# Optimization experiments

Hardware: AMD Instinct MI355X
Metric: run time of the kernel (lower is better)

Reference implementation:

```python
import jax, jax.numpy as jnp
import numpy as np

B, N, G = 1, 8192, 512      # batch, n_cells, n_genes
D_DEN = 512                  # denoise hidden
D_EMB1, D_EMB = 256, 32      # embed hidden / final embed dim
D_Q = 64                     # quality hidden
H = 4                        # interaction heads
LBD = 1.0


def _lin_init(key, fan_in, fan_out):
    # torch nn.Linear default init (uniform +/- 1/sqrt(fan_in)); stored as [in,out]
    k1, k2 = jax.random.split(key)
    bound = 1.0 / np.sqrt(fan_in)
    W = jax.random.uniform(k1, (fan_in, fan_out), minval=-bound, maxval=bound, dtype=jnp.float32)
    b = jax.random.uniform(k2, (fan_out,), minval=-bound, maxval=bound, dtype=jnp.float32)
    return W, b


def setup_inputs() -> dict:
    key = jax.random.key(0)
    ks = jax.random.split(key, 9)
    raw_expr = jax.random.normal(ks[0], (B, N, G), dtype=jnp.float32)
    dW1, db1 = _lin_init(ks[1], G, D_DEN)
    dW2, db2 = _lin_init(ks[2], D_DEN, G)
    eW1, eb1 = _lin_init(ks[3], G, D_EMB1)
    eW2, eb2 = _lin_init(ks[4], D_EMB1, D_EMB)
    qW1, qb1 = _lin_init(ks[5], G, D_Q)
    qW2, qb2 = _lin_init(ks[6], D_Q, 1)
    # CellInteract.transform: xavier_normal -> std = sqrt(2/(d+d)) = 1/sqrt(d)
    transforms = jax.random.normal(ks[7], (H, D_EMB, D_EMB), dtype=jnp.float32) * np.float32(1.0 / np.sqrt(D_EMB))
    # gene_response is a trained parameter (zeros at init); random so path is non-trivial
    gene_responses = jax.random.normal(ks[8], (H, G, G), dtype=jnp.float32) * np.float32(0.02)
    return dict(raw_expr=raw_expr, dW1=dW1, db1=db1, dW2=dW2, db2=db2,
                eW1=eW1, eb1=eb1, eW2=eW2, eb2=eb2,
                qW1=qW1, qb1=qb1, qW2=qW2, qb2=qb2,
                transforms=transforms, gene_responses=gene_responses)


def _cdist(x):
    # pairwise euclidean distance over cells: [B,N,D] -> [B,N,N], grad-safe at 0
    sq = jnp.sum(x * x, axis=-1)
    d2 = sq[..., :, None] + sq[..., None, :] - 2.0 * jnp.einsum('bnd,bmd->bnm', x, x)
    d2 = jnp.maximum(d2, 0.0)
    eps = 1e-12
    safe = jnp.where(d2 > eps, d2, eps)
    return jnp.where(d2 > eps, jnp.sqrt(safe), 0.0)


def reference(raw_expr, dW1, db1, dW2, db2, eW1, eb1, eW2, eb2,
              qW1, qb1, qW2, qb2, transforms, gene_responses):
    # CellDenoise: Linear-Tanh-Linear + residual
    denoised = jnp.tanh(raw_expr @ dW1 + db1) @ dW2 + db2 + raw_expr      # [B,N,G]
    # CellQualify: Linear-Tanh-Linear -> [B,N,1]
    quality = jnp.tanh(raw_expr @ qW1 + qb1) @ qW2 + qb2
    # CellEmbed: Linear-Tanh-Linear -> [B,N,D_EMB]
    enc = jnp.tanh(raw_expr @ eW1 + eb1) @ eW2 + eb2
    # CellSmooth: softmax(-cdist + quality^T) @ denoised
    scores = -_cdist(enc) + jnp.swapaxes(quality, -1, -2)                 # [B,N,N]
    sim = jax.nn.softmax(scores, axis=-1)
    smoothed = sim @ denoised                                             # [B,N,G]
    # CellInteract heads (interact=True path): sigmoid(enc T enc^T) @ expr @ gene_response / N
    inter = jnp.zeros_like(smoothed)
    for h in range(H):
        ci = jax.nn.sigmoid(jnp.einsum('bnd,de,bme->bnm', enc, transforms[h], enc))
        inter = inter + (ci @ smoothed) @ gene_responses[h] / N
    final = smoothed + LBD * inter
    return denoised, smoothed, final
```

## Files before the change

kernel.cpp:

```cpp
#include <hip/hip_runtime.h>
#include <hip/hip_bf16.h>
#include <stdint.h>
#if !__has_builtin(__builtin_amdgcn_cvt_pk_fp8_f32)
#include <hip/hip_fp8.h>
#endif

#define NC 8192
#define GG 512

typedef __attribute__((ext_vector_type(8))) short bf16x8;
typedef __attribute__((ext_vector_type(4))) float fx4;
typedef __attribute__((ext_vector_type(4))) unsigned int uint4v;
typedef __attribute__((ext_vector_type(2))) long long llx2;

__device__ __forceinline__ float bf2f(short s){
  union { uint32_t u; float f; } c; c.u = ((uint32_t)(uint16_t)s) << 16; return c.f;
}
__device__ __forceinline__ short f2bf(float f){
  union { float f; uint32_t u; } c; c.f = f;
  uint32_t u = c.u;
  uint32_t r = (u + 0x7fffu + ((u >> 16) & 1u)) >> 16;
  return (short)(uint16_t)r;
}
__device__ __forceinline__ uint32_t au(float f){
  union { float f; uint32_t u; } c; c.f = f; return c.u;
}
#if __has_builtin(__builtin_amdgcn_rcpf)
__device__ __forceinline__ float fast_rcp(float x){ return __builtin_amdgcn_rcpf(x); }
#else
__device__ __forceinline__ float fast_rcp(float x){ return 1.0f / x; }
#endif
#if __has_builtin(__builtin_amdgcn_sqrtf)
__device__ __forceinline__ float fast_sqrt(float x){ return __builtin_amdgcn_sqrtf(x); }
#else
__device__ __forceinline__ float fast_sqrt(float x){ return sqrtf(x); }
#endif
__device__ __forceinline__ float tanh_fast(float x){
  float e = __expf(2.0f * x);
  return 1.0f - 2.0f * fast_rcp(e + 1.0f);
}
__device__ __forceinline__ uint32_t pack_bf(float lo, float hi){
  return __builtin_amdgcn_perm(au(hi) + 0x8000u, au(lo) + 0x8000u, 0x07060302u);
}
template<bool HI>
__device__ __forceinline__ uint32_t pk_fp8(float a, float b, uint32_t old){
#if __has_builtin(__builtin_amdgcn_cvt_pk_fp8_f32)
  return (uint32_t)__builtin_amdgcn_cvt_pk_fp8_f32(a, b, (int)old, HI);
#else
  __hip_fp8_e4m3 fa(a), fb(b);
  uint32_t v = (uint32_t)fa.__x | ((uint32_t)fb.__x << 8);
  return HI ? ((old & 0x0000ffffu) | (v << 16)) : ((old & 0xffff0000u) | v);
#endif
}
__device__ __forceinline__ void g2l16(const void* g, void* l){
  __builtin_amdgcn_global_load_lds((const __attribute__((address_space(1))) void*)g,
                                   (__attribute__((address_space(3))) void*)l, 16, 0, 0);
}

__global__ void cast_f32_bf16(const float* __restrict__ in, short* __restrict__ out, int n){
  int i = (blockIdx.x * 256 + threadIdx.x) * 4;
  if (i < n){
    float4 v = *(const float4*)(in + i);
    uint32_t lo = (uint32_t)(uint16_t)f2bf(v.x) | ((uint32_t)(uint16_t)f2bf(v.y) << 16);
    uint32_t hi = (uint32_t)(uint16_t)f2bf(v.z) | ((uint32_t)(uint16_t)f2bf(v.w) << 16);
    *(uint2*)(out + i) = make_uint2(lo, hi);
  }
}

__global__ void transpose_cast(const float* __restrict__ in, short* __restrict__ out,
                               int R, int C, int ostride, int roff, int permute){
  __shared__ float t[32][33];
  int c0 = blockIdx.x * 32, r0 = blockIdx.y * 32;
  int x = threadIdx.x & 31, y = threadIdx.x >> 5;
  #pragma unroll
  for (int it = 0; it < 4; ++it)
    t[y + 8*it][x] = in[(size_t)(r0 + y + 8*it) * C + c0 + x];
  __syncthreads();
  int xp = permute ? (((x >> 2) & 3) * 8 + ((x >> 4) & 1) * 4 + (x & 3)) : x;
  #pragma unroll
  for (int it = 0; it < 4; ++it)
    out[(size_t)(c0 + y + 8*it) * ostride + roff + r0 + xp] = f2bf(t[x][y + 8*it]);
}

__global__ void transpose_cast8(const float* __restrict__ in, unsigned char* __restrict__ out,
                                int C, int ostride){
  __shared__ float t[32][33];
  int c0 = blockIdx.x * 32, r0 = blockIdx.y * 32;
  int x = threadIdx.x & 31, y = threadIdx.x >> 5;
  #pragma unroll
  for (int it = 0; it < 4; ++it)
    t[y + 8*it][x] = in[(size_t)(r0 + y + 8*it) * C + c0 + x];
  __syncthreads();
  int xp = ((x >> 2) & 3) * 16 + ((r0 >> 5) & 1) * 8 + ((x >> 4) & 1) * 4 + (x & 3);
  int cb = r0 & ~63;
  #pragma unroll
  for (int it = 0; it < 4; ++it){
    float v = t[x][y + 8*it];
    out[(size_t)(c0 + y + 8*it) * ostride + cb + xp] =
        (unsigned char)(pk_fp8<false>(v, v, 0u) & 0xffu);
  }
}

__global__ void fill_bias(const float* __restrict__ db1, const float* __restrict__ eb1,
                          const float* __restrict__ qb1, float* __restrict__ b){
  int i = blockIdx.x * 256 + threadIdx.x;
  if (i >= 896) return;
  float v = 0.0f;
  if (i < 512) v = db1[i];
  else if (i < 768) v = eb1[i - 512];
  else if (i < 832) v = qb1[i - 768];
  b[i] = v;
}

__global__ __launch_bounds__(256, 2)
void gemm_bt(const short* __restrict__ A, int lda, const short* __restrict__ B, int ldb,
             int K, int mode, const float* __restrict__ bias,
             const float* __restrict__ res, int ldres,
             float* __restrict__ outf, short* __restrict__ outb, int ldo, float scale)
{
  __shared__ __align__(16) short As[64 * 64];
  __shared__ __align__(16) short Bs[128 * 64];
  const int tid = threadIdx.x;
  const int lane = tid & 63, wave = tid >> 6;
  const int wm = wave >> 1, wn = wave & 1;
  const int l16 = lane & 15, q = lane >> 4;
  const size_t i0 = (size_t)blockIdx.y * 64;
  const int n0 = blockIdx.x * 128;
  fx4 acc[2][4] = {};

  for (int k0 = 0; k0 < K; k0 += 64){
    #pragma unroll
    for (int inst = 0; inst < 2; ++inst){
      int ch = inst * 256 + tid;
      int r = ch >> 3, pc = ch & 7;
      int colc = (pc ^ (r & 7)) * 8;
      g2l16(A + (i0 + r) * (size_t)lda + k0 + colc, As + ch * 8);
    }
    #pragma unroll
    for (int inst = 0; inst < 4; ++inst){
      int ch = inst * 256 + tid;
      int r = ch >> 3, pc = ch & 7;
      int colc = (pc ^ (r & 7)) * 8;
      g2l16(B + (size_t)(n0 + r) * (size_t)ldb + k0 + colc, Bs + ch * 8);
    }
    __syncthreads();
    #pragma unroll
    for (int ks = 0; ks < 2; ++ks){
      int k8 = ks * 4 + q;
      bf16x8 af[2], bfr[4];
      #pragma unroll
      for (int mi = 0; mi < 2; ++mi){
        int r = wm * 32 + mi * 16 + l16;
        af[mi] = *(const bf16x8*)(As + r * 64 + ((k8 ^ (r & 7)) << 3));
      }
      #pragma unroll
      for (int ni = 0; ni < 4; ++ni){
        int r = wn * 64 + ni * 16 + l16;
        bfr[ni] = *(const bf16x8*)(Bs + r * 64 + ((k8 ^ (r & 7)) << 3));
      }
      #pragma unroll
      for (int mi = 0; mi < 2; ++mi)
        #pragma unroll
        for (int ni = 0; ni < 4; ++ni)
          acc[mi][ni] = __builtin_amdgcn_mfma_f32_16x16x32_bf16(af[mi], bfr[ni], acc[mi][ni], 0, 0, 0);
    }
    __syncthreads();
  }
  #pragma unroll
  for (int mi = 0; mi < 2; ++mi){
    #pragma unroll
    for (int ni = 0; ni < 4; ++ni){
      int n = n0 + wn * 64 + ni * 16 + l16;
      float b = bias ? bias[n] : 0.0f;
      #pragma unroll
      for (int r = 0; r < 4; ++r){
        size_t m = i0 + wm * 32 + mi * 16 + q * 4 + r;
        float v = acc[mi][ni][r];
        size_t o = m * (size_t)ldo + n;
        if (mode == 0)      outb[o] = f2bf(tanh_fast(v + b));
        else if (mode == 1) outf[o] = v + b + res[m * (size_t)ldres + n];
        else                outf[o] += v * scale;
      }
    }
  }
}

template<int GT, int CH, int MODE, int ISL>
__global__ __launch_bounds__(256, (MODE == 0) ? 4 : 2)
void attn_reg(const short* __restrict__ encA, const short* __restrict__ encJ,
              const short* __restrict__ VTp,
              const float* __restrict__ sq, const float* __restrict__ E,
              float* __restrict__ out0, float* __restrict__ out1,
              short* __restrict__ outb, int ldo)
{
  constexpr int NG  = GT / 16;
  constexpr int KS  = CH / 32;
  constexpr int CPR = CH / 8;
  constexpr int SH  = (CPR == 4) ? 1 : 0;
  constexpr int HB  = GT * CH;
  __shared__ __align__(16) short Vl[2 * HB];
  const int tid = threadIdx.x, lane = tid & 63, wave = tid >> 6;
  const int l16 = lane & 15, q = lane >> 4;
  const int ib = blockIdx.y * (64 * ISL) + wave * 16;
  const int g0 = blockIdx.x * GT;
  const short* Ai = encA + (size_t)blockIdx.z * NC * 32;

  bf16x8 bi[ISL];
  float sqi[ISL], lacc[ISL];
  #pragma unroll
  for (int s = 0; s < ISL; ++s){
    bi[s] = *(const bf16x8*)(Ai + (size_t)(ib + s * 64 + l16) * 32 + q * 8);
    lacc[s] = 0.f;
    sqi[s] = (MODE == 0) ? sq[ib + s * 64 + l16] : 0.f;
  }
  fx4 acc[ISL][NG] = {};
  uint4v bP[ISL][KS], bPn[ISL][KS];

  auto stage = [&](int jc, int buf){
    #pragma unroll
    for (int inst = 0; inst < HB / 2048; ++inst){
      int ch = inst * 256 + tid;
      int r = ch / CPR, pc = ch % CPR;
      int colc = (pc ^ ((r >> SH) & (CPR - 1))) * 8;
      g2l16(VTp + (size_t)(g0 + r) * NC + jc + colc, Vl + buf * HB + ch * 8);
    }
  };
  auto transform = [&](int jb, uint4v (*o)[KS]){
    #pragma unroll
    for (int ks = 0; ks < KS; ++ks){
      uint32_t dw[ISL][4];
      #pragma unroll
      for (int jt = 0; jt < 2; ++jt){
        int j0t = jb + ks * 32 + jt * 16;
        bf16x8 aj = *(const bf16x8*)(encJ + (size_t)(j0t + l16) * 32 + q * 8);
        float4 sqj = {}, Ej = {};
        if (MODE == 0){
          sqj = *(const float4*)(sq + j0t + q * 4);
          Ej  = *(const float4*)(E  + j0t + q * 4);
        }
        #pragma unroll
        for (int s = 0; s < ISL; ++s){
          fx4 c = {};
          c = __builtin_amdgcn_mfma_f32_16x16x32_bf16(aj, bi[s], c, 0, 0, 0);
          float pv[4];
          #pragma unroll
          for (int r = 0; r < 4; ++r){
            float dot = c[r];
            if (MODE == 0){
              float d2 = fmaxf(sqi[s] + ((const float*)&sqj)[r] - 2.0f * dot, 0.0f);
              float p = ((const float*)&Ej)[r] * __expf(-fast_sqrt(d2));
              lacc[s] += p;
              pv[r] = p;
            } else {
              pv[r] = fast_rcp(1.0f + __expf(-dot));
            }
          }
          dw[s][jt * 2]     = pack_bf(pv[0], pv[1]);
          dw[s][jt * 2 + 1] = pack_bf(pv[2], pv[3]);
        }
      }
      #pragma unroll
      for (int s = 0; s < ISL; ++s){
        uint4v u = { dw[s][0], dw[s][1], dw[s][2], dw[s][3] };
        o[s][ks] = u;
      }
    }
  };
  auto pv_step = [&](int buf){
    #pragma unroll
    for (int ks = 0; ks < KS; ++ks){
      int k8 = ks * 4 + q;
      #pragma unroll
      for (int gt = 0; gt < NG; ++gt){
        int rr = gt * 16 + l16;
        bf16x8 av = *(const bf16x8*)(Vl + buf * HB + rr * CH +
                                     ((k8 ^ ((rr >> SH) & (CPR - 1))) << 3));
        #pragma unroll
        for (int s = 0; s < ISL; ++s)
          acc[s][gt] = __builtin_amdgcn_mfma_f32_16x16x32_bf16(
              av, *(const bf16x8*)&bP[s][ks], acc[s][gt], 0, 0, 0);
      }
    }
  };

  stage(0, 0);
  transform(0, bP);
  __syncthreads();
  for (int jc = 0; jc < NC; jc += CH){
    int buf = (jc / CH) & 1;
    int nxt = jc + CH;
    if (nxt < NC){
      stage(nxt, buf ^ 1);
      transform(nxt, bPn);
    }
    pv_step(buf);
    #pragma unroll
    for (int s = 0; s < ISL; ++s)
      #pragma unroll
      for (int ks = 0; ks < KS; ++ks) bP[s][ks] = bPn[s][ks];
    if (nxt < NC) __syncthreads();
  }

  #pragma unroll
  for (int s = 0; s < ISL; ++s){
    int irow = ib + s * 64 + l16;
    if (MODE == 0){
      float v = lacc[s];
      v += __shfl_xor(v, 16);
      v += __shfl_xor(v, 32);
      float inv = fast_rcp(v);
      #pragma unroll
      for (int gt = 0; gt < NG; ++gt){
        int g = g0 + gt * 16 + q * 4;
        float4 o;
        o.x = acc[s][gt][0] * inv; o.y = acc[s][gt][1] * inv;
        o.z = acc[s][gt][2] * inv; o.w = acc[s][gt][3] * inv;
        size_t off = (size_t)irow * GG + g;
        *(float4*)(out0 + off) = o;
        *(float4*)(out1 + off) = o;
      }
    } else {
      #pragma unroll
      for (int gt = 0; gt < NG; ++gt){
        int g = g0 + gt * 16 + q * 4;
        uint2 u;
        u.x = pack_bf(acc[s][gt][0], acc[s][gt][1]);
        u.y = pack_bf(acc[s][gt][2], acc[s][gt][3]);
        *(uint2*)(outb + (size_t)irow * ldo + (size_t)blockIdx.z * GG + g) = u;
      }
    }
  }
}

__global__ __launch_bounds__(256, 2)
void attn_f8(const short* __restrict__ encA, const short* __restrict__ encJ,
             const unsigned char* __restrict__ V8, short* __restrict__ outb, int ldo)
{
  __shared__ __align__(16) unsigned char Vl[2 * 512 * 64];
  __shared__ __align__(16) unsigned char Pl[2 * 4096];
  const int tid = threadIdx.x, lane = tid & 63, wave = tid >> 6;
  const int l16 = lane & 15, q = lane >> 4;
  const int i0 = blockIdx.y * 64;
  const short* Ai = encA + (size_t)blockIdx.z * NC * 32;
  const bf16x8 bi = *(const bf16x8*)(Ai + (size_t)(i0 + wave * 16 + l16) * 32 + q * 8);
  fx4 acc[4][8] = {};

  auto stage = [&](int jc, int buf){
    #pragma unroll
    for (int inst = 0; inst < 8; ++inst){
      int ch = inst * 256 + tid;
      int r = ch >> 2, pc = ch & 3;
      int colc = (pc ^ ((r >> 1) & 3)) * 16;
      g2l16(V8 + (size_t)r * NC + jc + colc, Vl + buf * 32768 + ch * 16);
    }
  };
  auto transform = [&](int jb, int buf){
    uint32_t dwa[2][2];
    #pragma unroll
    for (int ks = 0; ks < 2; ++ks){
      #pragma unroll
      for (int jt = 0; jt < 2; ++jt){
        int j0t = jb + ks * 32 + jt * 16;
        bf16x8 aj = *(const bf16x8*)(encJ + (size_t)(j0t + l16) * 32 + q * 8);
        fx4 c = {};
        c = __builtin_amdgcn_mfma_f32_16x16x32_bf16(aj, bi, c, 0, 0, 0);
        float p[4];
        #pragma unroll
        for (int r = 0; r < 4; ++r)
          p[r] = fast_rcp(1.0f + __expf(-c[r]));
        dwa[ks][jt] = pk_fp8<true>(p[2], p[3], pk_fp8<false>(p[0], p[1], 0u));
      }
    }
    uint4v u = { dwa[0][0], dwa[0][1], dwa[1][0], dwa[1][1] };
    *(uint4v*)(Pl + buf * 4096 + ((wave * 4 + q) * 16 + l16) * 16) = u;
  };
  auto pv_step = [&](int buf){
    llx2 pf[4];
    #pragma unroll
    for (int it = 0; it < 4; ++it)
      pf[it] = *(const llx2*)(Pl + buf * 4096 + ((it * 4 + q) * 16 + l16) * 16);
    #pragma unroll
    for (int gt = 0; gt < 8; ++gt){
      int rr = wave * 128 + gt * 16 + l16;
      llx2 av = *(const llx2*)(Vl + buf * 32768 + rr * 64 + ((q ^ ((rr >> 1) & 3)) << 4));
      #pragma unroll
      for (int it = 0; it < 4; ++it){
        acc[it][gt] = __builtin_amdgcn_mfma_f32_16x16x32_fp8_fp8(av[0], pf[it][0], acc[it][gt], 0, 0, 0);
        acc[it][gt] = __builtin_amdgcn_mfma_f32_16x16x32_fp8_fp8(av[1], pf[it][1], acc[it][gt], 0, 0, 0);
      }
    }
  };

  stage(0, 0);
  transform(0, 0);
  __syncthreads();
  for (int jc = 0; jc < NC; jc += 64){
    int buf = (jc >> 6) & 1;
    int nxt = jc + 64;
    if (nxt < NC){
      stage(nxt, buf ^ 1);
      transform(nxt, buf ^ 1);
    }
    pv_step(buf);
    if (nxt < NC) __syncthreads();
  }

  #pragma unroll
  for (int it = 0; it < 4; ++it){
    int irow = i0 + it * 16 + l16;
    #pragma unroll
    for (int gt = 0; gt < 8; ++gt){
      int g = wave * 128 + gt * 16 + q * 4;
      uint2 u;
      u.x = pack_bf(acc[it][gt][0], acc[it][gt][1]);
      u.y = pack_bf(acc[it][gt][2], acc[it][gt][3]);
      *(uint2*)(outb + (size_t)irow * ldo + (size_t)blockIdx.z * GG + g) = u;
    }
  }
}

__global__ void embed2_kernel(const short* __restrict__ H2, int lda,
                              const float* __restrict__ eW2,
                              const float* __restrict__ eb2, const float* __restrict__ T4,
                              short* __restrict__ encb, float* __restrict__ sq,
                              short* __restrict__ Ah)
{
  __shared__ float encS[8][32];
  int d = threadIdx.x & 31, cl = threadIdx.x >> 5;
  size_t c = (size_t)blockIdx.x * 8 + cl;
  float s = eb2[d];
  const short* hrow = H2 + c * lda;
  for (int k = 0; k < 256; ++k) s += bf2f(hrow[k]) * eW2[k * 32 + d];
  short eb = f2bf(s);
  encb[c * 32 + d] = eb;
  encS[cl][d] = bf2f(eb);
  __syncthreads();
  if (d == 0){
    float t = 0;
    for (int k = 0; k < 32; ++k) t += encS[cl][k] * encS[cl][k];
    sq[c] = t;
  }
  #pragma unroll
  for (int h = 0; h < 4; ++h){
    float a = 0;
    const float* T = T4 + h * 1024;
    for (int k = 0; k < 32; ++k) a += encS[cl][k] * T[k * 32 + d];
    Ah[(size_t)h * NC * 32 + c * 32 + d] = f2bf(a);
  }
}

__global__ void qtail_kernel(const short* __restrict__ Hq, int lda,
                             const float* __restrict__ qW2, const float* __restrict__ qb2,
                             float* __restrict__ E)
{
  int j = threadIdx.x & 63, cl = threadIdx.x >> 6;
  size_t c = (size_t)blockIdx.x * 4 + cl;
  float t = bf2f(Hq[c * lda + j]) * qW2[j];
  #pragma unroll
  for (int o = 32; o >= 1; o >>= 1) t += __shfl_xor(t, o);
  if (j == 0) E[c] = __expf(t + qb2[0]);
}

extern "C" void kernel_launch(void* const* d_in, const int* in_sizes, int n_in,
                              void* d_out, int out_size, void* d_ws, size_t ws_size,
                              hipStream_t stream)
{
  const float* raw = (const float*)d_in[0];
  const float* dW1 = (const float*)d_in[1];
  const float* db1 = (const float*)d_in[2];
  const float* dW2 = (const float*)d_in[3];
  const float* db2 = (const float*)d_in[4];
  const float* eW1 = (const float*)d_in[5];
  const float* eb1 = (const float*)d_in[6];
  const float* eW2 = (const float*)d_in[7];
  const float* eb2 = (const float*)d_in[8];
  const float* qW1 = (const float*)d_in[9];
  const float* qb1 = (const float*)d_in[10];
  const float* qW2 = (const float*)d_in[11];
  const float* qb2 = (const float*)d_in[12];
  const float* Tr  = (const float*)d_in[13];
  const float* Gr  = (const float*)d_in[14];

  float* outD = (float*)d_out;
  float* outS = outD + (size_t)NC * GG;
  float* outF = outS + (size_t)NC * GG;

  char* ws = (char*)d_ws;
  size_t off = 0;
  auto take = [&](size_t bytes) -> char* {
    char* p = ws + off; off += (bytes + 255) & ~(size_t)255; return p;
  };
  short* Xb    = (short*)take((size_t)NC * GG * 2);
  short* WcatT = (short*)take((size_t)896 * 512 * 2);
  short* dW2T  = (short*)take((size_t)512 * 512 * 2);
  short* GTc   = (short*)take((size_t)512 * 2048 * 2);
  float* bcat  = (float*)take((size_t)896 * 4);
  short* Hcat  = (short*)take((size_t)NC * 896 * 2);
  short* denTp = (short*)take((size_t)GG * NC * 2);
  unsigned char* smoT8 = (unsigned char*)take((size_t)GG * NC);
  short* encb  = (short*)take((size_t)NC * 32 * 2);
  short* Ahb   = (short*)take((size_t)4 * NC * 32 * 2);
  float* sqv   = (float*)take((size_t)NC * 4);
  float* Ev    = (float*)take((size_t)NC * 4);
  short* Ucat  = (short*)take((size_t)NC * 2048 * 2);

  dim3 b256(256);
  cast_f32_bf16<<<dim3((NC * GG) / 1024), b256, 0, stream>>>(raw, Xb, NC * GG);
  transpose_cast<<<dim3(16, 16), b256, 0, stream>>>(dW1, WcatT, 512, 512, 512, 0, 0);
  transpose_cast<<<dim3(8, 16),  b256, 0, stream>>>(eW1, WcatT + 512 * 512, 512, 256, 512, 0, 0);
  transpose_cast<<<dim3(2, 16),  b256, 0, stream>>>(qW1, WcatT + 768 * 512, 512, 64, 512, 0, 0);
  transpose_cast<<<dim3(16, 16), b256, 0, stream>>>(dW2, dW2T, 512, 512, 512, 0, 0);
  for (int h = 0; h < 4; ++h)
    transpose_cast<<<dim3(16, 16), b256, 0, stream>>>(Gr + (size_t)h * 512 * 512,
                                                      GTc, 512, 512, 2048, h * 512, 0);
  fill_bias<<<dim3(4), b256, 0, stream>>>(db1, eb1, qb1, bcat);
  gemm_bt<<<dim3(7, 128), b256, 0, stream>>>(Xb, 512, WcatT, 512, 512, 0, bcat,
                                             (const float*)nullptr, 0,
                                             (float*)nullptr, Hcat, 896, 1.0f);
  gemm_bt<<<dim3(4, 128), b256, 0, stream>>>(Hcat, 896, dW2T, 512, 512, 1, db2,
                                             raw, 512, outD, (short*)nullptr, 512, 1.0f);
  transpose_cast<<<dim3(16, 256), b256, 0, stream>>>(outD, denTp, NC, 512, NC, 0, 1);
  embed2_kernel<<<dim3(NC / 8), b256, 0, stream>>>(Hcat + 512, 896, eW2, eb2, Tr,
                                                   encb, sqv, Ahb);
  qtail_kernel<<<dim3(NC / 4), b256, 0, stream>>>(Hcat + 768, 896, qW2, qb2, Ev);
  attn_reg<128, 64, 0, 1><<<dim3(4, 128, 1), b256, 0, stream>>>(
      encb, encb, denTp, sqv, Ev, outS, outF, (short*)nullptr, 0);
  transpose_cast8<<<dim3(16, 256), b256, 0, stream>>>(outS, smoT8, 512, NC);
  attn_f8<<<dim3(1, 128, 4), b256, 0, stream>>>(Ahb, encb, smoT8, Ucat, 2048);
  gemm_bt<<<dim3(4, 128), b256, 0, stream>>>(Ucat, 2048, GTc, 2048, 2048,
                                             3, (const float*)nullptr,
                                             (const float*)nullptr, 0,
                                             outF, (short*)nullptr, 512, 1.0f / NC);
}
```

Measured before the change: 720.8 us.

## Split smoothing attention over key dimension with partial-sum combine kernel

The softmax-weighted smoothing kernel now splits the cell (key) loop across two grid slices, each writing unnormalized partial outputs and row sums into scratch space aliased onto the Ucat buffer. A new combine kernel adds the two partials, normalizes by the summed denominators, and writes both outputs. This doubles the number of blocks to improve CU occupancy, at the cost of an extra 32MB partial write/read pass and an additional launch.

```diff
diff --git a/kernel.cpp b/kernel.cpp
--- a/kernel.cpp
+++ b/kernel.cpp
@@ -65,6 +65,20 @@
     uint32_t hi = (uint32_t)(uint16_t)f2bf(v.z) | ((uint32_t)(uint16_t)f2bf(v.w) << 16);
     *(uint2*)(out + i) = make_uint2(lo, hi);
   }
+}
+
+__global__ void combine_smooth(const float* __restrict__ Po, const float* __restrict__ Ls,
+                               float* __restrict__ out0, float* __restrict__ out1){
+  size_t idx = ((size_t)blockIdx.x * 256 + threadIdx.x) * 4;
+  float4 a = *(const float4*)(Po + idx);
+  float4 b = *(const float4*)(Po + (size_t)NC * GG + idx);
+  int row = (int)(idx >> 9);
+  float inv = fast_rcp(Ls[row] + Ls[NC + row]);
+  float4 o;
+  o.x = (a.x + b.x) * inv; o.y = (a.y + b.y) * inv;
+  o.z = (a.z + b.z) * inv; o.w = (a.w + b.w) * inv;
+  *(float4*)(out0 + idx) = o;
+  *(float4*)(out1 + idx) = o;
 }
 
 __global__ void transpose_cast(const float* __restrict__ in, short* __restrict__ out,
@@ -203,7 +217,9 @@
   const int l16 = lane & 15, q = lane >> 4;
   const int ib = blockIdx.y * (64 * ISL) + wave * 16;
   const int g0 = blockIdx.x * GT;
-  const short* Ai = encA + (size_t)blockIdx.z * NC * 32;
+  const short* Ai = encA + (MODE == 1 ? (size_t)blockIdx.z * NC * 32 : (size_t)0);
+  const int jlen = NC / (int)gridDim.z;
+  const int jbase = (int)blockIdx.z * jlen;
 
   bf16x8 bi[ISL];
   float sqi[ISL], lacc[ISL];
@@ -283,22 +299,22 @@
     }
   };
 
-  stage(0, 0);
-  transform(0, bP);
+  stage(jbase, 0);
+  transform(jbase, bP);
   __syncthreads();
-  for (int jc = 0; jc < NC; jc += CH){
-    int buf = (jc / CH) & 1;
-    int nxt = jc + CH;
-    if (nxt < NC){
-      stage(nxt, buf ^ 1);
-      transform(nxt, bPn);
+  for (int t = 0; t < jlen; t += CH){
+    int buf = (t / CH) & 1;
+    int nt = t + CH;
+    if (nt < jlen){
+      stage(jbase + nt, buf ^ 1);
+      transform(jbase + nt, bPn);
     }
     pv_step(buf);
     #pragma unroll
     for (int s = 0; s < ISL; ++s)
       #pragma unroll
       for (int ks = 0; ks < KS; ++ks) bP[s][ks] = bPn[s][ks];
-    if (nxt < NC) __syncthreads();
+    if (nt < jlen) __syncthreads();
   }
 
   #pragma unroll
@@ -308,16 +324,14 @@
       float v = lacc[s];
       v += __shfl_xor(v, 16);
       v += __shfl_xor(v, 32);
-      float inv = fast_rcp(v);
+      if (g0 == 0 && q == 0) out1[(size_t)blockIdx.z * NC + irow] = v;
       #pragma unroll
       for (int gt = 0; gt < NG; ++gt){
         int g = g0 + gt * 16 + q * 4;
         float4 o;
-        o.x = acc[s][gt][0] * inv; o.y = acc[s][gt][1] * inv;
-        o.z = acc[s][gt][2] * inv; o.w = acc[s][gt][3] * inv;
-        size_t off = (size_t)irow * GG + g;
-        *(float4*)(out0 + off) = o;
-        *(float4*)(out1 + off) = o;
+        o.x = acc[s][gt][0]; o.y = acc[s][gt][1];
+        o.z = acc[s][gt][2]; o.w = acc[s][gt][3];
+        *(float4*)(out0 + ((size_t)blockIdx.z * NC + irow) * GG + g) = o;
       }
     } else {
       #pragma unroll
@@ -502,7 +516,9 @@
   short* Ahb   = (short*)take((size_t)4 * NC * 32 * 2);
   float* sqv   = (float*)take((size_t)NC * 4);
   float* Ev    = (float*)take((size_t)NC * 4);
+  float* Lsum  = (float*)take((size_t)2 * NC * 4);
   short* Ucat  = (short*)take((size_t)NC * 2048 * 2);
+  float* Po    = (float*)Ucat;
 
   dim3 b256(256);
   cast_f32_bf16<<<dim3((NC * GG) / 1024), b256, 0, stream>>>(raw, Xb, NC * GG);
@@ -523,8 +539,9 @@
   embed2_kernel<<<dim3(NC / 8), b256, 0, stream>>>(Hcat + 512, 896, eW2, eb2, Tr,
                                                    encb, sqv, Ahb);
   qtail_kernel<<<dim3(NC / 4), b256, 0, stream>>>(Hcat + 768, 896, qW2, qb2, Ev);
-  attn_reg<128, 64, 0, 1><<<dim3(4, 128, 1), b256, 0, stream>>>(
-      encb, encb, denTp, sqv, Ev, outS, outF, (short*)nullptr, 0);
+  attn_reg<128, 64, 0, 1><<<dim3(4, 128, 2), b256, 0, stream>>>(
+      encb, encb, denTp, sqv, Ev, Po, Lsum, (short*)nullptr, 0);
+  combine_smooth<<<dim3((NC * GG) / 1024), b256, 0, stream>>>(Po, Lsum, outS, outF);
   transpose_cast8<<<dim3(16, 256), b256, 0, stream>>>(outS, smoT8, 512, NC);
   attn_f8<<<dim3(1, 128, 4), b256, 0, stream>>>(Ahb, encb, smoT8, Ucat, 2048);
   gemm_bt<<<dim3(4, 128), b256, 0, stream>>>(Ucat, 2048, GTc, 2048, 2048,
```

Result: faster. 675.9 us (-6.2%).
